# Kernel optimization log

Hardware: AMD Instinct MI355X
Metric: run time of the kernel (lower is better)

Reference implementation:

```python
import jax, jax.numpy as jnp
import numpy as np

N, L, D = 32768, 15, 256
VOCAB, SCORE_MAX = 27, 100


def setup_inputs() -> dict:
    key = jax.random.key(0)
    ks = jax.random.split(key, 16)
    inp = {
        'words': jax.random.randint(ks[0], (N, L), 0, VOCAB, dtype=jnp.int32),
        'rows': jax.random.randint(ks[1], (N,), 0, L, dtype=jnp.int32),
        'cols': jax.random.randint(ks[2], (N,), 0, L, dtype=jnp.int32),
        'dirs': jax.random.randint(ks[3], (N,), 0, 2, dtype=jnp.int32),
        'scores': jax.random.randint(ks[4], (N,), 0, 150, dtype=jnp.int32),
        'letter_emb': jax.random.normal(ks[5], (VOCAB, D), jnp.float32),
        'positional': jax.random.normal(ks[6], (L, D), jnp.float32),
        'Wq': jax.random.normal(ks[7], (D, D), jnp.float32) / np.sqrt(D),
        'bq': jax.random.normal(ks[8], (D,), jnp.float32) * 0.01,
        'Wk': jax.random.normal(ks[9], (D, D), jnp.float32) / np.sqrt(D),
        'bk': jax.random.normal(ks[10], (D,), jnp.float32) * 0.01,
        'Wv': jax.random.normal(ks[11], (D, D), jnp.float32) / np.sqrt(D),
        'bv': jax.random.normal(ks[12], (D,), jnp.float32) * 0.01,
        'row_emb': jax.random.normal(ks[13], (L, D), jnp.float32),
        'col_emb': jax.random.normal(ks[14], (L, D), jnp.float32),
        'dir_emb': jax.random.normal(ks[15], (2, D), jnp.float32),
        'score_emb': jax.random.normal(jax.random.fold_in(key, 99), (SCORE_MAX, D), jnp.float32),
    }
    return inp


def reference(words, rows, cols, dirs, scores, letter_emb, positional, Wq, bq, Wk, bk, Wv, bv, row_emb, col_emb, dir_emb, score_emb):
    # WordEncoder: letter embedding + positional, then single-head self-attention, sum over positions
    emb = letter_emb[words] + positional[None, :, :]            # [N, L, D]
    q = emb @ Wq.T + bq                                          # [N, L, D]
    k = emb @ Wk.T + bk
    v = emb @ Wv.T + bv
    att = jax.nn.softmax(jnp.einsum('nld,nmd->nlm', q, k), axis=-1)  # [N, L, L]
    word = jnp.einsum('nlm,nmd->nd', att, v)                     # (att @ v).sum(axis=1) -> [N, D]
    # VectorEncoder
    vector = row_emb[rows] + col_emb[cols] + dir_emb[dirs]       # [N, D]
    # score embedding (clamped to score_max - 1)
    score_v = score_emb[jnp.minimum(scores, SCORE_MAX - 1)]      # [N, D]
    # original computes word_enc(move.word) twice (word + ordered) -> 2 * word
    return 2.0 * word + vector + score_v
```

## Files before the change

kernel.cpp:

```cpp
#include <hip/hip_runtime.h>
#include <hip/hip_bf16.h>

#define NMOV 32768
#define LW 15
#define DIM 256
#define NVOC 27
#define NR 405
#define GSH 408
#define MPB 16

__device__ __forceinline__ float b2f(unsigned short u) {
    return __uint_as_float(((unsigned int)u) << 16);
}

__device__ const unsigned char PAIR_LUT[120] = {
    0x00,
    0x10,0x11,
    0x20,0x21,0x22,
    0x30,0x31,0x32,0x33,
    0x40,0x41,0x42,0x43,0x44,
    0x50,0x51,0x52,0x53,0x54,0x55,
    0x60,0x61,0x62,0x63,0x64,0x65,0x66,
    0x70,0x71,0x72,0x73,0x74,0x75,0x76,0x77,
    0x80,0x81,0x82,0x83,0x84,0x85,0x86,0x87,0x88,
    0x90,0x91,0x92,0x93,0x94,0x95,0x96,0x97,0x98,0x99,
    0xA0,0xA1,0xA2,0xA3,0xA4,0xA5,0xA6,0xA7,0xA8,0xA9,0xAA,
    0xB0,0xB1,0xB2,0xB3,0xB4,0xB5,0xB6,0xB7,0xB8,0xB9,0xBA,0xBB,
    0xC0,0xC1,0xC2,0xC3,0xC4,0xC5,0xC6,0xC7,0xC8,0xC9,0xCA,0xCB,0xCC,
    0xD0,0xD1,0xD2,0xD3,0xD4,0xD5,0xD6,0xD7,0xD8,0xD9,0xDA,0xDB,0xDC,0xDD,
    0xE0,0xE1,0xE2,0xE3,0xE4,0xE5,0xE6,0xE7,0xE8,0xE9,0xEA,0xEB,0xEC,0xED,0xEE
};

__global__ __launch_bounds__(256) void qkv_gemm(
    const float* __restrict__ le, const float* __restrict__ pos,
    const float* __restrict__ Wq, const float* __restrict__ bq,
    const float* __restrict__ Wk, const float* __restrict__ bk,
    const float* __restrict__ Wv, const float* __restrict__ bv,
    float* __restrict__ QT, float* __restrict__ KT,
    __hip_bfloat16* __restrict__ VT)
{
    __shared__ float Ash[16][260];
    __shared__ float Bsh[16][260];
    const int t  = threadIdx.x;
    const int bx = blockIdx.x % 48;
    const int by = blockIdx.x / 48;
    const int r0 = by * 16;
    const int mat = bx >> 4;
    const int nb  = (bx & 15) * 16;
    const float* W  = (mat == 0) ? Wq : (mat == 1) ? Wk : Wv;
    const float* bb = (mat == 0) ? bq : (mat == 1) ? bk : bv;

    #pragma unroll
    for (int s = 0; s < 4; ++s) {
        int slot = s * 256 + t;
        int row = slot >> 6, q4 = slot & 63;
        int r = r0 + row;
        float4 va = make_float4(0.f, 0.f, 0.f, 0.f);
        if (r < NR) {
            int c = r / 15, l = r - c * 15;
            float4 lv = *(const float4*)&le[c * DIM + q4 * 4];
            float4 pv = *(const float4*)&pos[l * DIM + q4 * 4];
            va = make_float4(lv.x + pv.x, lv.y + pv.y, lv.z + pv.z, lv.w + pv.w);
        }
        *(float4*)&Ash[row][q4 * 4] = va;
        float4 vb = *(const float4*)&W[(nb + row) * DIM + q4 * 4];
        *(float4*)&Bsh[row][q4 * 4] = vb;
    }
    __syncthreads();

    const int tj = t & 15, ti = t >> 4;
    float acc = 0.f;
    #pragma unroll 8
    for (int k = 0; k < DIM; k += 4) {
        float4 a = *(const float4*)&Ash[ti][k];
        float4 b = *(const float4*)&Bsh[tj][k];
        acc += a.x * b.x + a.y * b.y + a.z * b.z + a.w * b.w;
    }

    const int r = r0 + ti;
    if (r < NR) {
        float v = acc + bb[nb + tj];
        int dcol = nb + tj;
        if (mat == 0)      QT[r * DIM + dcol] = v;
        else if (mat == 1) KT[r * DIM + dcol] = v;
        else               VT[r * DIM + dcol] = __float2bfloat16(v);
    }
}

__global__ __launch_bounds__(256) void h_matrix(
    const float* __restrict__ QT, const float* __restrict__ KT,
    float2* __restrict__ H)
{
    __shared__ float Qi[16][68], Ki[16][68], Qj[16][68], Kj[16][68];

    int rem = blockIdx.x, bi = 0, cnt = 26;
    while (rem >= cnt) { rem -= cnt; ++bi; --cnt; }
    const int bj = bi + rem;
    const int i0 = bi * 16, j0 = bj * 16;
    const int t = threadIdx.x;
    const int ti = t >> 4, tj = t & 15;

    float acc_ij = 0.f, acc_ji = 0.f;

    for (int k0 = 0; k0 < DIM; k0 += 64) {
        #pragma unroll
        for (int s = 0; s < 4; ++s) {
            int slot = s * 256 + t;
            int tile = slot >> 8;
            int r    = (slot >> 4) & 15;
            int c4   = slot & 15;
            int grow = (tile < 2) ? (i0 + r) : (j0 + r);
            const float* src = (tile == 0 || tile == 2) ? QT : KT;
            float4 v = (grow < NR)
                ? *(const float4*)&src[grow * DIM + k0 + c4 * 4]
                : make_float4(0.f, 0.f, 0.f, 0.f);
            float* dst = (tile == 0) ? &Qi[r][c4 * 4]
                       : (tile == 1) ? &Ki[r][c4 * 4]
                       : (tile == 2) ? &Qj[r][c4 * 4] : &Kj[r][c4 * 4];
            *(float4*)dst = v;
        }
        __syncthreads();
        #pragma unroll 4
        for (int k = 0; k < 64; k += 4) {
            float4 qi = *(const float4*)&Qi[ti][k];
            float4 kj = *(const float4*)&Kj[tj][k];
            float4 qj = *(const float4*)&Qj[ti][k];
            float4 ki = *(const float4*)&Ki[tj][k];
            acc_ij += qi.x * kj.x + qi.y * kj.y + qi.z * kj.z + qi.w * kj.w;
            acc_ji += qj.x * ki.x + qj.y * ki.y + qj.z * ki.z + qj.w * ki.w;
        }
        __syncthreads();
    }

    Qi[ti][tj] = acc_ij;
    Ki[ti][tj] = acc_ji;
    __syncthreads();
    const float t_ij = Qi[tj][ti];
    const float t_ji = Ki[tj][ti];

    const int i1 = i0 + ti, j1 = j0 + tj;
    if (i1 < NR && j1 < NR) H[i1 * GSH + j1] = make_float2(acc_ij, t_ji);
    const int i2 = j0 + ti, j2 = i0 + tj;
    if (i2 < NR && j2 < NR) H[i2 * GSH + j2] = make_float2(acc_ji, t_ij);
}

__global__ __launch_bounds__(256) void moves_kernel(
    const int* __restrict__ words, const int* __restrict__ rowsI,
    const int* __restrict__ colsI, const int* __restrict__ dirsI,
    const int* __restrict__ scoresI,
    const float2* __restrict__ H, const __hip_bfloat16* __restrict__ VT,
    const float* __restrict__ row_emb, const float* __restrict__ col_emb,
    const float* __restrict__ dir_emb, const float* __restrict__ score_emb,
    float* __restrict__ out)
{
    __shared__ float S[MPB][LW][17];
    __shared__ int   rIdx[MPB][16];
    __shared__ float csum[MPB][16];
    __shared__ int   meta[MPB][4];
    const int base = blockIdx.x * MPB;
    const int t  = threadIdx.x;
    const int w  = t >> 6;
    const int ln = t & 63;
    const int hw = t >> 5;
    const int j  = t & 31;

    if (ln < 60) {
        int mvl = ln / 15, row = ln - mvl * 15;
        int mv = w * 4 + mvl;
        rIdx[mv][row] = words[(base + mv) * LW + row] * LW + row;
    }
    if (ln < 16) {
        int mvl = ln >> 2, f = ln & 3;
        int n = base + w * 4 + mvl;
        int v = (f == 0) ? rowsI[n] : (f == 1) ? colsI[n]
              : (f == 2) ? dirsI[n] : min(scoresI[n], 99);
        meta[w * 4 + mvl][f] = v;
    }
    __builtin_amdgcn_wave_barrier();

    const int mv0 = hw * 2, mv1 = mv0 + 1;
    float2 h0[4], h1[4];
    int ll[4], mm[4];
    #pragma unroll
    for (int k = 0; k < 4; ++k) {
        int p = j + 32 * k;
        if (p < 120) {
            int lm = PAIR_LUT[p];
            ll[k] = lm >> 4; mm[k] = lm & 15;
            h0[k] = H[(size_t)rIdx[mv0][ll[k]] * GSH + rIdx[mv0][mm[k]]];
            h1[k] = H[(size_t)rIdx[mv1][ll[k]] * GSH + rIdx[mv1][mm[k]]];
        }
    }
    #pragma unroll
    for (int k = 0; k < 4; ++k) {
        int p = j + 32 * k;
        if (p < 120) {
            S[mv0][ll[k]][mm[k]] = h0[k].x;
            S[mv0][mm[k]][ll[k]] = h0[k].y;
            S[mv1][ll[k]][mm[k]] = h1[k].x;
            S[mv1][mm[k]][ll[k]] = h1[k].y;
        }
    }
    __builtin_amdgcn_wave_barrier();

    if (ln < 60) {
        int mvl = ln / 15, row = ln - mvl * 15;
        int mv = w * 4 + mvl;
        float s[LW];
        #pragma unroll
        for (int m = 0; m < LW; ++m) s[m] = S[mv][row][m];
        float mx = s[0];
        #pragma unroll
        for (int m = 1; m < LW; ++m) mx = fmaxf(mx, s[m]);
        float sum = 0.f;
        #pragma unroll
        for (int m = 0; m < LW; ++m) { s[m] = __expf(s[m] - mx); sum += s[m]; }
        float inv = 1.0f / sum;
        #pragma unroll
        for (int m = 0; m < LW; ++m) S[mv][row][m] = s[m] * inv;
    }
    __builtin_amdgcn_wave_barrier();

    if (ln < 60) {
        int mvl = ln / 15, col = ln - mvl * 15;
        int mv = w * 4 + mvl;
        float acc = 0.f;
        #pragma unroll
        for (int l = 0; l < LW; ++l) acc += S[mv][l][col];
        csum[mv][col] = acc;
    }
    __builtin_amdgcn_wave_barrier();

    const int d0 = ln * 4;
    const unsigned short* VT16 = (const unsigned short*)VT;
    #pragma unroll 1
    for (int s2 = 0; s2 < 4; ++s2) {
        const int i = w * 4 + s2;
        const int n = base + i;
        float4 re = *(const float4*)&row_emb[meta[i][0] * DIM + d0];
        float4 ce = *(const float4*)&col_emb[meta[i][1] * DIM + d0];
        float4 de = *(const float4*)&dir_emb[meta[i][2] * DIM + d0];
        float4 se = *(const float4*)&score_emb[meta[i][3] * DIM + d0];
        ushort4 va[8];
        #pragma unroll
        for (int m = 0; m < 8; ++m)
            va[m] = *(const ushort4*)(VT16 + (size_t)rIdx[i][m] * DIM + d0);
        float wx = 0.f, wy = 0.f, wz = 0.f, ww = 0.f;
        #pragma unroll
        for (int m = 0; m < 8; ++m) {
            float c = csum[i][m];
            wx += c * b2f(va[m].x); wy += c * b2f(va[m].y);
            wz += c * b2f(va[m].z); ww += c * b2f(va[m].w);
        }
        ushort4 vb[7];
        #pragma unroll
        for (int m = 0; m < 7; ++m)
            vb[m] = *(const ushort4*)(VT16 + (size_t)rIdx[i][8 + m] * DIM + d0);
        #pragma unroll
        for (int m = 0; m < 7; ++m) {
            float c = csum[i][8 + m];
            wx += c * b2f(vb[m].x); wy += c * b2f(vb[m].y);
            wz += c * b2f(vb[m].z); ww += c * b2f(vb[m].w);
        }
        float4 res;
        res.x = 2.f * wx + re.x + ce.x + de.x + se.x;
        res.y = 2.f * wy + re.y + ce.y + de.y + se.y;
        res.z = 2.f * wz + re.z + ce.z + de.z + se.z;
        res.w = 2.f * ww + re.w + ce.w + de.w + se.w;
        *(float4*)&out[(size_t)n * DIM + d0] = res;
    }
}

extern "C" void kernel_launch(void* const* d_in, const int* in_sizes, int n_in,
                              void* d_out, int out_size, void* d_ws, size_t ws_size,
                              hipStream_t stream)
{
    const int*   words      = (const int*)d_in[0];
    const int*   rowsI      = (const int*)d_in[1];
    const int*   colsI      = (const int*)d_in[2];
    const int*   dirsI      = (const int*)d_in[3];
    const int*   scoresI    = (const int*)d_in[4];
    const float* letter_emb = (const float*)d_in[5];
    const float* positional = (const float*)d_in[6];
    const float* Wq         = (const float*)d_in[7];
    const float* bq         = (const float*)d_in[8];
    const float* Wk         = (const float*)d_in[9];
    const float* bk         = (const float*)d_in[10];
    const float* Wv         = (const float*)d_in[11];
    const float* bv         = (const float*)d_in[12];
    const float* row_emb    = (const float*)d_in[13];
    const float* col_emb    = (const float*)d_in[14];
    const float* dir_emb    = (const float*)d_in[15];
    const float* score_emb  = (const float*)d_in[16];
    float* out = (float*)d_out;

    float*  QT = (float*)d_ws;
    float*  KT = QT + NR * DIM;
    float2* Hm = (float2*)(KT + NR * DIM);
    __hip_bfloat16* VT = (__hip_bfloat16*)((char*)Hm + (size_t)NR * GSH * sizeof(float2));

    qkv_gemm<<<26 * 48, 256, 0, stream>>>(letter_emb, positional, Wq, bq, Wk, bk,
                                          Wv, bv, QT, KT, VT);
    h_matrix<<<351, 256, 0, stream>>>(QT, KT, Hm);
    moves_kernel<<<NMOV / MPB, 256, 0, stream>>>(words, rowsI, colsI, dirsI,
                                                 scoresI, Hm, VT, row_emb,
                                                 col_emb, dir_emb, score_emb,
                                                 out);
}
```

Before: 63.20 us.

## Retile QKV GEMM, pack epilogue embeddings to bf16, hoist H gathers

The QKV projection kernel now uses 32x32 output tiles with K-chunked shared memory and a 2x2 register micro-tile. Extra blocks in the same launch convert the row, column, direction and score embedding tables into one bf16 table. The moves kernel reads that packed bf16 table instead of four fp32 tables, which halves epilogue gather bytes at the cost of bf16 rounding of the embedding values. It also issues the H-matrix gathers straight from the word indices before the shared-index setup, so those loads can start earlier.

Result: slower. 65.23 us (+3.2%).

```diff
diff --git a/kernel.cpp b/kernel.cpp
--- a/kernel.cpp
+++ b/kernel.cpp
@@ -11,6 +11,10 @@
 
 __device__ __forceinline__ float b2f(unsigned short u) {
     return __uint_as_float(((unsigned int)u) << 16);
+}
+__device__ __forceinline__ unsigned short f2bu(float x) {
+    __hip_bfloat16 h = __float2bfloat16(x);
+    return *reinterpret_cast<unsigned short*>(&h);
 }
 
 __device__ const unsigned char PAIR_LUT[120] = {
@@ -36,54 +40,87 @@
     const float* __restrict__ Wq, const float* __restrict__ bq,
     const float* __restrict__ Wk, const float* __restrict__ bk,
     const float* __restrict__ Wv, const float* __restrict__ bv,
+    const float* __restrict__ row_emb, const float* __restrict__ col_emb,
+    const float* __restrict__ dir_emb, const float* __restrict__ score_emb,
     float* __restrict__ QT, float* __restrict__ KT,
-    __hip_bfloat16* __restrict__ VT)
+    __hip_bfloat16* __restrict__ VT, __hip_bfloat16* __restrict__ EPI)
 {
-    __shared__ float Ash[16][260];
-    __shared__ float Bsh[16][260];
-    const int t  = threadIdx.x;
-    const int bx = blockIdx.x % 48;
-    const int by = blockIdx.x / 48;
-    const int r0 = by * 16;
-    const int mat = bx >> 4;
-    const int nb  = (bx & 15) * 16;
+    const int t = threadIdx.x;
+    if (blockIdx.x >= 312) {
+        int idx = (blockIdx.x - 312) * 1024 + t * 4;
+        float4 v;
+        if (idx < 15 * 256)       v = *(const float4*)&row_emb[idx];
+        else if (idx < 30 * 256)  v = *(const float4*)&col_emb[idx - 15 * 256];
+        else if (idx < 32 * 256)  v = *(const float4*)&dir_emb[idx - 30 * 256];
+        else                      v = *(const float4*)&score_emb[idx - 32 * 256];
+        ushort4 o;
+        o.x = f2bu(v.x); o.y = f2bu(v.y); o.z = f2bu(v.z); o.w = f2bu(v.w);
+        *(ushort4*)((unsigned short*)EPI + idx) = o;
+        return;
+    }
+
+    __shared__ float Ash[32][68];
+    __shared__ float Bsh[32][68];
+    const int bx = blockIdx.x % 24;
+    const int by = blockIdx.x / 24;
+    const int r0 = by * 32;
+    const int mat = bx >> 3;
+    const int nb  = (bx & 7) * 32;
     const float* W  = (mat == 0) ? Wq : (mat == 1) ? Wk : Wv;
     const float* bb = (mat == 0) ? bq : (mat == 1) ? bk : bv;
 
+    const int ti = t >> 4, tj = t & 15;
+    float acc00 = 0.f, acc01 = 0.f, acc10 = 0.f, acc11 = 0.f;
+
+    for (int k0 = 0; k0 < DIM; k0 += 64) {
+        #pragma unroll
+        for (int s = 0; s < 2; ++s) {
+            int slot = s * 256 + t;
+            int row = slot >> 4, c4 = slot & 15;
+            int r = r0 + row;
+            float4 va = make_float4(0.f, 0.f, 0.f, 0.f);
+            if (r < NR) {
+                int c = r / 15, l = r - c * 15;
+                float4 lv = *(const float4*)&le[c * DIM + k0 + c4 * 4];
+                float4 pv = *(const float4*)&pos[l * DIM + k0 + c4 * 4];
+                va = make_float4(lv.x + pv.x, lv.y + pv.y, lv.z + pv.z, lv.w + pv.w);
+            }
+            *(float4*)&Ash[row][c4 * 4] = va;
+            float4 vb = *(const float4*)&W[(nb + row) * DIM + k0 + c4 * 4];
+            *(float4*)&Bsh[row][c4 * 4] = vb;
+        }
+        __syncthreads();
+        #pragma unroll 4
+        for (int kk = 0; kk < 64; kk += 4) {
+            float4 a0 = *(const float4*)&Ash[2 * ti][kk];
+            float4 a1 = *(const float4*)&Ash[2 * ti + 1][kk];
+            float4 b0 = *(const float4*)&Bsh[tj][kk];
+            float4 b1 = *(const float4*)&Bsh[tj + 16][kk];
+            acc00 += a0.x * b0.x + a0.y * b0.y + a0.z * b0.z + a0.w * b0.w;
+            acc01 += a0.x * b1.x + a0.y * b1.y + a0.z * b1.z + a0.w * b1.w;
+            acc10 += a1.x * b0.x + a1.y * b0.y + a1.z * b0.z + a1.w * b0.w;
+            acc11 += a1.x * b1.x + a1.y * b1.y + a1.z * b1.z + a1.w * b1.w;
+        }
+        __syncthreads();
+    }
+
+    const int c0 = nb + tj, c1 = nb + tj + 16;
+    const float bias0 = bb[c0], bias1 = bb[c1];
     #pragma unroll
-    for (int s = 0; s < 4; ++s) {
-        int slot = s * 256 + t;
-        int row = slot >> 6, q4 = slot & 63;
-        int r = r0 + row;
-        float4 va = make_float4(0.f, 0.f, 0.f, 0.f);
+    for (int rr = 0; rr < 2; ++rr) {
+        int r = r0 + 2 * ti + rr;
         if (r < NR) {
-            int c = r / 15, l = r - c * 15;
-            float4 lv = *(const float4*)&le[c * DIM + q4 * 4];
-            float4 pv = *(const float4*)&pos[l * DIM + q4 * 4];
-            va = make_float4(lv.x + pv.x, lv.y + pv.y, lv.z + pv.z, lv.w + pv.w);
-        }
-        *(float4*)&Ash[row][q4 * 4] = va;
-        float4 vb = *(const float4*)&W[(nb + row) * DIM + q4 * 4];
-        *(float4*)&Bsh[row][q4 * 4] = vb;
-    }
-    __syncthreads();
-
-    const int tj = t & 15, ti = t >> 4;
-    float acc = 0.f;
-    #pragma unroll 8
-    for (int k = 0; k < DIM; k += 4) {
-        float4 a = *(const float4*)&Ash[ti][k];
-        float4 b = *(const float4*)&Bsh[tj][k];
-        acc += a.x * b.x + a.y * b.y + a.z * b.z + a.w * b.w;
-    }
-
-    const int r = r0 + ti;
-    if (r < NR) {
-        float v = acc + bb[nb + tj];
-        int dcol = nb + tj;
-        if (mat == 0)      QT[r * DIM + dcol] = v;
-        else if (mat == 1) KT[r * DIM + dcol] = v;
-        else               VT[r * DIM + dcol] = __float2bfloat16(v);
+            float v0 = (rr == 0 ? acc00 : acc10) + bias0;
+            float v1 = (rr == 0 ? acc01 : acc11) + bias1;
+            if (mat == 0) {
+                QT[r * DIM + c0] = v0; QT[r * DIM + c1] = v1;
+            } else if (mat == 1) {
+                KT[r * DIM + c0] = v0; KT[r * DIM + c1] = v1;
+            } else {
+                VT[r * DIM + c0] = __float2bfloat16(v0);
+                VT[r * DIM + c1] = __float2bfloat16(v1);
+            }
+        }
     }
 }
 
@@ -149,8 +186,7 @@
     const int* __restrict__ colsI, const int* __restrict__ dirsI,
     const int* __restrict__ scoresI,
     const float2* __restrict__ H, const __hip_bfloat16* __restrict__ VT,
-    const float* __restrict__ row_emb, const float* __restrict__ col_emb,
-    const float* __restrict__ dir_emb, const float* __restrict__ score_emb,
+    const __hip_bfloat16* __restrict__ EPI,
     float* __restrict__ out)
 {
     __shared__ float S[MPB][LW][17];
@@ -164,33 +200,39 @@
     const int hw = t >> 5;
     const int j  = t & 31;
 
-    if (ln < 60) {
-        int mvl = ln / 15, row = ln - mvl * 15;
-        int mv = w * 4 + mvl;
-        rIdx[mv][row] = words[(base + mv) * LW + row] * LW + row;
-    }
-    if (ln < 16) {
-        int mvl = ln >> 2, f = ln & 3;
-        int n = base + w * 4 + mvl;
-        int v = (f == 0) ? rowsI[n] : (f == 1) ? colsI[n]
-              : (f == 2) ? dirsI[n] : min(scoresI[n], 99);
-        meta[w * 4 + mvl][f] = v;
-    }
-    __builtin_amdgcn_wave_barrier();
-
     const int mv0 = hw * 2, mv1 = mv0 + 1;
+    const int* w0 = words + (base + mv0) * LW;
+    const int* w1 = words + (base + mv1) * LW;
+    int ll[4], mm[4];
     float2 h0[4], h1[4];
-    int ll[4], mm[4];
     #pragma unroll
     for (int k = 0; k < 4; ++k) {
         int p = j + 32 * k;
         if (p < 120) {
             int lm = PAIR_LUT[p];
             ll[k] = lm >> 4; mm[k] = lm & 15;
-            h0[k] = H[(size_t)rIdx[mv0][ll[k]] * GSH + rIdx[mv0][mm[k]]];
-            h1[k] = H[(size_t)rIdx[mv1][ll[k]] * GSH + rIdx[mv1][mm[k]]];
-        }
-    }
+            int rl0 = w0[ll[k]] * LW + ll[k];
+            int rm0 = w0[mm[k]] * LW + mm[k];
+            int rl1 = w1[ll[k]] * LW + ll[k];
+            int rm1 = w1[mm[k]] * LW + mm[k];
+            h0[k] = H[(size_t)rl0 * GSH + rm0];
+            h1[k] = H[(size_t)rl1 * GSH + rm1];
+        }
+    }
+
+    if (ln < 60) {
+        int mvl = ln / 15, row = ln - mvl * 15;
+        int mv = w * 4 + mvl;
+        rIdx[mv][row] = words[(base + mv) * LW + row] * LW + row;
+    }
+    if (ln < 16) {
+        int mvl = ln >> 2, f = ln & 3;
+        int n = base + w * 4 + mvl;
+        int v = (f == 0) ? rowsI[n] : (f == 1) ? 15 + colsI[n]
+              : (f == 2) ? 30 + dirsI[n] : 32 + min(scoresI[n], 99);
+        meta[w * 4 + mvl][f] = v;
+    }
+
     #pragma unroll
     for (int k = 0; k < 4; ++k) {
         int p = j + 32 * k;
@@ -233,14 +275,15 @@
 
     const int d0 = ln * 4;
     const unsigned short* VT16 = (const unsigned short*)VT;
+    const unsigned short* EP16 = (const unsigned short*)EPI;
     #pragma unroll 1
     for (int s2 = 0; s2 < 4; ++s2) {
         const int i = w * 4 + s2;
         const int n = base + i;
-        float4 re = *(const float4*)&row_emb[meta[i][0] * DIM + d0];
-        float4 ce = *(const float4*)&col_emb[meta[i][1] * DIM + d0];
-        float4 de = *(const float4*)&dir_emb[meta[i][2] * DIM + d0];
-        float4 se = *(const float4*)&score_emb[meta[i][3] * DIM + d0];
+        ushort4 re = *(const ushort4*)(EP16 + meta[i][0] * DIM + d0);
+        ushort4 ce = *(const ushort4*)(EP16 + meta[i][1] * DIM + d0);
+        ushort4 de = *(const ushort4*)(EP16 + meta[i][2] * DIM + d0);
+        ushort4 se = *(const ushort4*)(EP16 + meta[i][3] * DIM + d0);
         ushort4 va[8];
         #pragma unroll
         for (int m = 0; m < 8; ++m)
@@ -263,10 +306,10 @@
             wz += c * b2f(vb[m].z); ww += c * b2f(vb[m].w);
         }
         float4 res;
-        res.x = 2.f * wx + re.x + ce.x + de.x + se.x;
-        res.y = 2.f * wy + re.y + ce.y + de.y + se.y;
-        res.z = 2.f * wz + re.z + ce.z + de.z + se.z;
-        res.w = 2.f * ww + re.w + ce.w + de.w + se.w;
+        res.x = 2.f * wx + b2f(re.x) + b2f(ce.x) + b2f(de.x) + b2f(se.x);
+        res.y = 2.f * wy + b2f(re.y) + b2f(ce.y) + b2f(de.y) + b2f(se.y);
+        res.z = 2.f * wz + b2f(re.z) + b2f(ce.z) + b2f(de.z) + b2f(se.z);
+        res.w = 2.f * ww + b2f(re.w) + b2f(ce.w) + b2f(de.w) + b2f(se.w);
         *(float4*)&out[(size_t)n * DIM + d0] = res;
     }
 }
@@ -297,13 +340,13 @@
     float*  QT = (float*)d_ws;
     float*  KT = QT + NR * DIM;
     float2* Hm = (float2*)(KT + NR * DIM);
-    __hip_bfloat16* VT = (__hip_bfloat16*)((char*)Hm + (size_t)NR * GSH * sizeof(float2));
-
-    qkv_gemm<<<26 * 48, 256, 0, stream>>>(letter_emb, positional, Wq, bq, Wk, bk,
-                                          Wv, bv, QT, KT, VT);
+    __hip_bfloat16* VT  = (__hip_bfloat16*)((char*)Hm + (size_t)NR * GSH * sizeof(float2));
+    __hip_bfloat16* EPI = VT + (size_t)NR * DIM;
+
+    qkv_gemm<<<345, 256, 0, stream>>>(letter_emb, positional, Wq, bq, Wk, bk,
+                                      Wv, bv, row_emb, col_emb, dir_emb,
+                                      score_emb, QT, KT, VT, EPI);
     h_matrix<<<351, 256, 0, stream>>>(QT, KT, Hm);
     moves_kernel<<<NMOV / MPB, 256, 0, stream>>>(words, rowsI, colsI, dirsI,
-                                                 scoresI, Hm, VT, row_emb,
-                                                 col_emb, dir_emb, score_emb,
-                                                 out);
-}
+                                                 scoresI, Hm, VT, EPI, out);
+}
```
